# Kernel optimization log

Measured on AMD Instinct MI355X. Metric: run time of the kernel, lower is better.

The kernel has to match this reference:

```python
import jax, jax.numpy as jnp
import numpy as np

H = 16           # num_heads
D = 1024         # num_units
QD = KD = VD = 64
LN_EPS = 1e-5


def _xavier(key, shape):
    fan_in, fan_out = shape[-2], shape[-1]
    std = np.sqrt(2.0 / (fan_in + fan_out))
    return jax.random.normal(key, shape, dtype=jnp.float32) * std


def setup_inputs() -> dict:
    key = jax.random.key(0)
    ks = jax.random.split(key, 10)
    B, Sq, Sk = 8, 1024, 1024
    return {
        "query": jax.random.normal(ks[0], (B, Sq, D), dtype=jnp.float32),
        "keys": jax.random.normal(ks[1], (B, Sk, D), dtype=jnp.float32),
        "values": jax.random.normal(ks[2], (B, Sk, D), dtype=jnp.float32),
        "Wq": _xavier(ks[3], (H, D, QD)),
        "Wk": _xavier(ks[4], (H, D, KD)),
        "Wv": _xavier(ks[5], (H, D, VD)),
        "Wp": _xavier(ks[6], (H * VD, D)),   # proj, stored input-major: y = x @ Wp + bp
        "bp": jnp.zeros((D,), dtype=jnp.float32),
        "gamma": jnp.ones((D,), dtype=jnp.float32),
        "beta": jnp.zeros((D,), dtype=jnp.float32),
    }


def reference(query, keys, values, Wq, Wk, Wv, Wp, bp, gamma, beta):
    B, Sq, _ = query.shape
    Sk = keys.shape[1]
    # RepeatLinear per head: [B,S,D] x [H,D,e] -> [H,B,S,e]
    Q = jnp.einsum("bsd,hde->hbse", query, Wq)
    K = jnp.einsum("bsd,hde->hbse", keys, Wk)
    V = jnp.einsum("bsd,hde->hbse", values, Wv)
    # NOTE: original scales by sqrt(num_units), not sqrt(key_dim)
    temper = jnp.asarray(np.sqrt(D), dtype=Q.dtype)
    scores = jnp.einsum("hbqe,hbke->hbqk", Q, K) / temper  # [H,B,Sq,Sk]
    attn = jax.nn.softmax(scores, axis=-1)
    # dropout is identity in eval mode
    out = jnp.einsum("hbqk,hbke->hbqe", attn, V)           # [H,B,Sq,VD]
    # torch.cat(torch.split(out, B, 0), -1): head-major feature concat
    out = out.transpose(1, 2, 0, 3).reshape(B, Sq, H * VD)
    out = out @ Wp + bp                                     # proj
    # residual + LayerNorm
    y = out + query
    mu = jnp.mean(y, axis=-1, keepdims=True)
    var = jnp.var(y, axis=-1, keepdims=True)
    y = (y - mu) / jnp.sqrt(var + LN_EPS) * gamma + beta
    return y, attn.reshape(H * B, Sq, Sk)
```

## Files before the change

### kernel.cpp

```cpp
#include <hip/hip_runtime.h>
#include <hip/hip_bf16.h>

#define H_ 16
#define B_ 8
#define S_ 1024
#define D_ 1024
#define E_ 64
#define HB_ 128
#define LN_EPS 1e-5f

typedef unsigned short u16;
typedef __bf16 bf16x8 __attribute__((ext_vector_type(8)));
typedef u16 u16x8 __attribute__((ext_vector_type(8)));
typedef u16 u16x4 __attribute__((ext_vector_type(4)));
typedef float f32x4 __attribute__((ext_vector_type(4)));

#define MFMA16(a, b, c) __builtin_amdgcn_mfma_f32_16x16x32_bf16( \
    __builtin_bit_cast(bf16x8, (a)), __builtin_bit_cast(bf16x8, (b)), (c), 0, 0, 0)

#define GLL16(gp, lp) __builtin_amdgcn_global_load_lds( \
    (const __attribute__((address_space(1))) void*)(gp), \
    (__attribute__((address_space(3))) void*)(lp), 16, 0, 0)

__device__ __forceinline__ u16 f2bf(float x) {
  union { float f; unsigned u; } v; v.f = x;
  unsigned r = v.u + 0x7fffu + ((v.u >> 16) & 1u);
  return (u16)(r >> 16);
}

__global__ __launch_bounds__(256) void k_transpose_all(
    const float* __restrict__ Wq, const float* __restrict__ Wk,
    const float* __restrict__ Wv, const float* __restrict__ Wp,
    u16* __restrict__ Wt) {
  __shared__ float tile[64][65];
  const int bid = blockIdx.x;
  const int which = bid >> 8, r = bid & 255;
  const float* src;
  int R, C, rt, ct;
  float scale = 1.0f;
  size_t soff, doff;
  if (which < 3) {
    src = which == 0 ? Wq : which == 1 ? Wk : Wv;
    if (which == 0) scale = 1.0f / 32.0f;
    int slice = r & 15, rtile = r >> 4;
    R = 1024; C = 64; rt = rtile * 64; ct = 0;
    soff = (size_t)slice * 65536;
    doff = (size_t)which * (1 << 20) + (size_t)slice * 65536;
  } else {
    src = Wp;
    R = 1024; C = 1024; rt = (r & 15) * 64; ct = (r >> 4) * 64;
    soff = 0; doff = (size_t)3 * (1 << 20);
  }
  const float* I = src + soff;
  u16* O = Wt + doff;
  const int t = threadIdx.x;
  const int c4 = (t & 15) * 4;
  #pragma unroll
  for (int i = 0; i < 4; i++) {
    int rr = i * 16 + (t >> 4);
    f32x4 v = *(const f32x4*)&I[(size_t)(rt + rr) * C + ct + c4];
    tile[rr][c4 + 0] = v[0]; tile[rr][c4 + 1] = v[1];
    tile[rr][c4 + 2] = v[2]; tile[rr][c4 + 3] = v[3];
  }
  __syncthreads();
  #pragma unroll
  for (int i = 0; i < 4; i++) {
    int oc = i * 16 + (t >> 4);
    u16x4 v;
    #pragma unroll
    for (int rr = 0; rr < 4; rr++) v[rr] = f2bf(tile[c4 + rr][oc] * scale);
    *(u16x4*)&O[(size_t)(ct + oc) * R + rt + c4] = v;
  }
}

__global__ void k_convert3(const float* __restrict__ Xq, const float* __restrict__ Xk,
    const float* __restrict__ Xv, u16* __restrict__ dst) {
  const int bid = blockIdx.x;
  const int t = bid >> 12;
  const float* X = t == 0 ? Xq : t == 1 ? Xk : Xv;
  u16* Y = dst + (size_t)t * (8 << 20);
  int i = ((bid & 4095) * 256 + threadIdx.x) * 8;
  float4 a = *(const float4*)(X + i);
  float4 b = *(const float4*)(X + i + 4);
  u16x8 v;
  v[0] = f2bf(a.x); v[1] = f2bf(a.y); v[2] = f2bf(a.z); v[3] = f2bf(a.w);
  v[4] = f2bf(b.x); v[5] = f2bf(b.y); v[6] = f2bf(b.z); v[7] = f2bf(b.w);
  *(u16x8*)(Y + i) = v;
}

#define STAGE_TILES() do { \
    GLL16(Ag + kt,             AsB0); \
    GLL16(Ag + 64 * 1024 + kt, AsB0 + 2048); \
    GLL16(Bg + kt,             BsB0); \
    GLL16(Bg + 64 * 1024 + kt, BsB0 + 2048); \
  } while (0)

#define READ_FRAGS() do { \
    _Pragma("unroll") \
    for (int mi = 0; mi < 4; mi++) \
      af[mi] = *(const u16x8*)&As[(wr * 64 + mi * 16 + lr) * 32 + lg * 8]; \
    _Pragma("unroll") \
    for (int ni = 0; ni < 4; ni++) \
      bf[ni] = *(const u16x8*)&Bs[(wc * 64 + ni * 16 + lr) * 32 + lg * 8]; \
  } while (0)

template<int MODE>
__global__ __launch_bounds__(256) void k_gemm(
    const u16* __restrict__ X0, const u16* __restrict__ Ball,
    u16* __restrict__ O0, u16* __restrict__ O1, u16* __restrict__ O2,
    float* __restrict__ Pf, const float* __restrict__ bp,
    const float* __restrict__ query) {
  const int bid = blockIdx.x + (blockIdx.y << 6);
  const int bx  = ((bid & 7) << 3) + ((bid >> 3) & 7);
  const int by  = bid >> 6;
  const int l  = threadIdx.x & 63;
  const int w  = threadIdx.x >> 6;
  const int lr = l & 15, lg = l >> 4;
  const int wr = w >> 1, wc = w & 1;
  const int m0 = bx * 128, n0 = by * 128;

  const u16* A = (MODE == 0) ? X0 + (size_t)(by >> 3) * (8 << 20) : X0;

  __shared__ __align__(16) u16 As[128 * 32];
  __shared__ __align__(16) u16 Bs[128 * 32];

  const int srow = w * 16 + (l >> 2);
  const int scol = (l & 3) * 8;
  const u16* Ag = A    + (size_t)(m0 + srow) * 1024 + scol;
  const u16* Bg = Ball + (size_t)(n0 + srow) * 1024 + scol;
  u16* AsB0 = As + w * 512;
  u16* BsB0 = Bs + w * 512;

  f32x4 acc[4][4] = {};
  u16x8 af[4], bf[4];

  if (MODE == 2 || by < 16) {
    for (int kt = 0; kt < 1024; kt += 32) {
      STAGE_TILES();
      __syncthreads();
      READ_FRAGS();
      #pragma unroll
      for (int mi = 0; mi < 4; mi++)
        #pragma unroll
        for (int ni = 0; ni < 4; ni++)
          acc[mi][ni] = MFMA16(bf[ni], af[mi], acc[mi][ni]);
      __syncthreads();
    }
  } else {
    for (int kt = 0; kt < 1024; kt += 32) {
      STAGE_TILES();
      __syncthreads();
      READ_FRAGS();
      #pragma unroll
      for (int mi = 0; mi < 4; mi++)
        #pragma unroll
        for (int ni = 0; ni < 4; ni++)
          acc[mi][ni] = MFMA16(af[mi], bf[ni], acc[mi][ni]);
      __syncthreads();
    }
  }

  if (MODE == 0 && by < 16) {
    u16* Out = (by >= 8) ? O1 : O0;
    const int h = (by & 7) * 2 + wc;
    #pragma unroll
    for (int mi = 0; mi < 4; mi++) {
      int s = m0 + wr * 64 + mi * 16 + lr;
      int bb = s >> 10, ss = s & 1023;
      #pragma unroll
      for (int ni = 0; ni < 4; ni++) {
        u16x4 v;
        #pragma unroll
        for (int r = 0; r < 4; r++) v[r] = f2bf(acc[mi][ni][r]);
        *(u16x4*)&Out[((size_t)(h * 8 + bb) * 1024 + ss) * 64 + ni * 16 + lg * 4] = v;
      }
    }
  } else if (MODE == 0) {
    const int byv = by - 16;
    const int h = byv * 2 + wc;
    #pragma unroll
    for (int mi = 0; mi < 4; mi++) {
      int s = m0 + wr * 64 + mi * 16 + lg * 4;
      int bb = s >> 10, ss = s & 1023;
      #pragma unroll
      for (int ni = 0; ni < 4; ni++) {
        u16x4 v;
        #pragma unroll
        for (int r = 0; r < 4; r++) v[r] = f2bf(acc[mi][ni][r]);
        *(u16x4*)&O2[((size_t)(h * 8 + bb) * 64 + ni * 16 + lr) * 1024 + ss] = v;
      }
    }
  } else {
    #pragma unroll
    for (int mi = 0; mi < 4; mi++) {
      int m = m0 + wr * 64 + mi * 16 + lr;
      #pragma unroll
      for (int ni = 0; ni < 4; ni++) {
        int n = n0 + wc * 64 + ni * 16 + lg * 4;
        f32x4 b4 = *(const f32x4*)(bp + n);
        f32x4 q4 = *(const f32x4*)(query + (size_t)m * 1024 + n);
        f32x4 o = acc[mi][ni] + b4 + q4;
        *(f32x4*)(Pf + (size_t)m * 1024 + n) = o;
      }
    }
  }
}

__global__ __launch_bounds__(256, 4) void k_attn(const u16* __restrict__ Qb,
    const u16* __restrict__ Kb, const u16* __restrict__ Vtb,
    float* __restrict__ attn_out, u16* __restrict__ AO) {
  const int bid = blockIdx.x;
  const int xcd = bid & 7, within = bid >> 3;
  const int qt = within & 63;
  const int hb = xcd * 16 + (within >> 6);
  const int w  = threadIdx.x >> 6;
  const int l  = threadIdx.x & 63;
  const int lr = l & 15, lg = l >> 4;
  const int q0 = qt * 16;

  __shared__ __align__(16) u16 pbuf[16 * 1024];
  __shared__ float wmaxs[4][16];
  __shared__ float wsums[4][16];

  const u16* Qp = Qb + ((size_t)hb * 1024 + q0 + lr) * 64 + lg * 8;
  const u16* Kp = Kb + ((size_t)hb * 1024 + w * 256 + lr) * 64 + lg * 8;
  u16x8 q_lo = *(const u16x8*)Qp;
  u16x8 q_hi = *(const u16x8*)(Qp + 32);

  f32x4 sacc[16] = {};
  __builtin_amdgcn_s_setprio(1);
  #pragma unroll
  for (int j = 0; j < 16; j++) {
    u16x8 k0 = *(const u16x8*)(Kp + (size_t)j * 16 * 64);
    u16x8 k1 = *(const u16x8*)(Kp + (size_t)j * 16 * 64 + 32);
    sacc[j] = MFMA16(k0, q_lo, sacc[j]);
    sacc[j] = MFMA16(k1, q_hi, sacc[j]);
  }
  __builtin_amdgcn_s_setprio(0);

  float mx = sacc[0][0];
  #pragma unroll
  for (int j = 0; j < 16; j++)
    #pragma unroll
    for (int r = 0; r < 4; r++) mx = fmaxf(mx, sacc[j][r]);
  mx = fmaxf(mx, __shfl_xor(mx, 16));
  mx = fmaxf(mx, __shfl_xor(mx, 32));

  float sum = 0.f;
  #pragma unroll
  for (int j = 0; j < 16; j++)
    #pragma unroll
    for (int r = 0; r < 4; r++) {
      float p = __expf(sacc[j][r] - mx);
      sacc[j][r] = p;
      sum += p;
    }
  sum += __shfl_xor(sum, 16);
  sum += __shfl_xor(sum, 32);

  const u16* Vp = Vtb + ((size_t)hb * 64 + w * 16 + lr) * 1024 + lg * 8;
  u16x8 vp0 = *(const u16x8*)(Vp + 0);
  u16x8 vp1 = *(const u16x8*)(Vp + 32);
  u16x8 vp2 = *(const u16x8*)(Vp + 64);
  u16x8 vp3 = *(const u16x8*)(Vp + 96);

  #pragma unroll
  for (int j = 0; j < 16; j++) {
    u16x4 pb;
    #pragma unroll
    for (int r = 0; r < 4; r++) pb[r] = f2bf(sacc[j][r]);
    int k0 = w * 256 + j * 16 + lg * 4;
    int byte = (lr * 2048 + k0 * 2) ^ ((lr & 7) << 4);
    *(u16x4*)((char*)pbuf + byte) = pb;
  }
  if (l < 16) { wmaxs[w][lr] = mx; wsums[w][lr] = sum; }

  __syncthreads();

  float m0v = wmaxs[0][lr], m1v = wmaxs[1][lr], m2v = wmaxs[2][lr], m3v = wmaxs[3][lr];
  float gmax = fmaxf(fmaxf(m0v, m1v), fmaxf(m2v, m3v));
  float e0 = __expf(m0v - gmax), e1 = __expf(m1v - gmax);
  float e2 = __expf(m2v - gmax), e3 = __expf(m3v - gmax);
  float gsum = wsums[0][lr] * e0 + wsums[1][lr] * e1 + wsums[2][lr] * e2 + wsums[3][lr] * e3;
  float inv = 1.0f / gsum;
  float c0 = e0 * inv, c1 = e1 * inv, c2 = e2 * inv, c3 = e3 * inv;
  float scale_own = __expf(mx - gmax) * inv;

  float* Ap = attn_out + ((size_t)hb * 1024 + q0 + lr) * 1024 + w * 256 + lg * 4;
  #pragma unroll
  for (int j = 0; j < 16; j++) {
    f32x4 v = sacc[j] * scale_own;
    __builtin_nontemporal_store(v, (f32x4*)(Ap + j * 16));
  }

  f32x4 o0 = {}, o1 = {}, o2 = {}, o3 = {};
  __builtin_amdgcn_s_setprio(1);
  #pragma unroll
  for (int i = 0; i < 4; i++)
    #pragma unroll
    for (int kk = 0; kk < 8; kk++) {
      int kb = i * 256 + kk * 32 + lg * 8;
      int byte = (lr * 2048 + kb * 2) ^ ((lr & 7) << 4);
      u16x8 p = *(u16x8*)((char*)pbuf + byte);
      u16x8 v;
      if (i == 0 && kk == 0) v = vp0;
      else if (i == 0 && kk == 1) v = vp1;
      else if (i == 0 && kk == 2) v = vp2;
      else if (i == 0 && kk == 3) v = vp3;
      else v = *(const u16x8*)(Vp + i * 256 + kk * 32);
      if (i == 0) o0 = MFMA16(v, p, o0);
      else if (i == 1) o1 = MFMA16(v, p, o1);
      else if (i == 2) o2 = MFMA16(v, p, o2);
      else o3 = MFMA16(v, p, o3);
    }
  __builtin_amdgcn_s_setprio(0);

  const int bb = hb & 7, hh = hb >> 3;
  u16x4 ov;
  #pragma unroll
  for (int r = 0; r < 4; r++)
    ov[r] = f2bf(o0[r] * c0 + o1[r] * c1 + o2[r] * c2 + o3[r] * c3);
  *(u16x4*)&AO[((size_t)bb * 1024 + q0 + lr) * 1024 + hh * 64 + w * 16 + lg * 4] = ov;
}

__global__ __launch_bounds__(256) void k_ln(const float* __restrict__ P,
    const float* __restrict__ gamma, const float* __restrict__ beta,
    float* __restrict__ y) {
  const int row = blockIdx.x * 4 + (threadIdx.x >> 6);
  const int l = threadIdx.x & 63;
  const float* p = P + (size_t)row * 1024 + l * 4;
  f32x4 v[4];
  float s = 0.f, s2 = 0.f;
  #pragma unroll
  for (int i = 0; i < 4; i++) {
    v[i] = *(const f32x4*)(p + i * 256);
    #pragma unroll
    for (int r = 0; r < 4; r++) { s += v[i][r]; s2 += v[i][r] * v[i][r]; }
  }
  #pragma unroll
  for (int off = 1; off < 64; off <<= 1) {
    s += __shfl_xor(s, off);
    s2 += __shfl_xor(s2, off);
  }
  float mu = s * (1.0f / 1024.0f);
  float var = s2 * (1.0f / 1024.0f) - mu * mu;
  float rstd = rsqrtf(var + LN_EPS);
  float* yp = y + (size_t)row * 1024 + l * 4;
  #pragma unroll
  for (int i = 0; i < 4; i++) {
    f32x4 g = *(const f32x4*)(gamma + l * 4 + i * 256);
    f32x4 b = *(const f32x4*)(beta + l * 4 + i * 256);
    f32x4 o;
    #pragma unroll
    for (int r = 0; r < 4; r++) o[r] = (v[i][r] - mu) * rstd * g[r] + b[r];
    __builtin_nontemporal_store(o, (f32x4*)(yp + i * 256));
  }
}

extern "C" void kernel_launch(void* const* d_in, const int* in_sizes, int n_in,
                              void* d_out, int out_size, void* d_ws, size_t ws_size,
                              hipStream_t stream) {
  const float* query  = (const float*)d_in[0];
  const float* keys   = (const float*)d_in[1];
  const float* values = (const float*)d_in[2];
  const float* Wq     = (const float*)d_in[3];
  const float* Wk     = (const float*)d_in[4];
  const float* Wv     = (const float*)d_in[5];
  const float* Wp     = (const float*)d_in[6];
  const float* bp     = (const float*)d_in[7];
  const float* gamma  = (const float*)d_in[8];
  const float* beta   = (const float*)d_in[9];

  float* y        = (float*)d_out;
  float* attn_out = (float*)d_out + (size_t)B_ * S_ * D_;

  u16* ws  = (u16*)d_ws;
  u16* Wqt = ws;
  u16* Wvt = Wqt + (2 << 20);
  u16* Wpt = Wqt + (3 << 20);
  u16* Xqb = Wqt + (4 << 20);
  u16* Xvb = Xqb + (16 << 20);
  u16* Qb  = Xqb + (24 << 20);
  u16* Kb  = Qb + (8 << 20);
  u16* Vtb = Kb + (8 << 20);
  u16* AO  = Vtb + (8 << 20);
  float* P = (float*)Xqb;
  (void)Wvt;

  k_transpose_all<<<1024, 256, 0, stream>>>(Wq, Wk, Wv, Wp, Wqt);
  k_convert3<<<12288, 256, 0, stream>>>(query, keys, values, Xqb);

  k_gemm<0><<<dim3(64, 24), 256, 0, stream>>>(Xqb, Wqt, Qb, Kb, Vtb, nullptr, nullptr, nullptr);

  k_attn<<<8192, 256, 0, stream>>>(Qb, Kb, Vtb, attn_out, AO);

  k_gemm<2><<<dim3(64, 8), 256, 0, stream>>>(AO, Wpt, nullptr, nullptr, nullptr, P, bp, query);
  k_ln<<<2048, 256, 0, stream>>>(P, gamma, beta, y);
}
```

Measured before the change: 421.9 us.

## Split attention into score/softmax kernel and separate tiled P·V GEMM

Splits the fused attention kernel into two. The first computes scores and softmax, then writes both the fp32 attention output and a bf16 copy of the probabilities to workspace. The second kernel runs P·V as a tiled GEMM using LDS loads. This removes each block's repeated V read and its large LDS staging buffer, but adds a full bf16 probability round trip through global memory plus an extra launch.

```diff
diff --git a/kernel.cpp b/kernel.cpp
--- a/kernel.cpp
+++ b/kernel.cpp
@@ -206,9 +206,8 @@
   }
 }
 
-__global__ __launch_bounds__(256, 4) void k_attn(const u16* __restrict__ Qb,
-    const u16* __restrict__ Kb, const u16* __restrict__ Vtb,
-    float* __restrict__ attn_out, u16* __restrict__ AO) {
+__global__ __launch_bounds__(256, 4) void k_score(const u16* __restrict__ Qb,
+    const u16* __restrict__ Kb, float* __restrict__ attn_out, u16* __restrict__ Pws) {
   const int bid = blockIdx.x;
   const int xcd = bid & 7, within = bid >> 3;
   const int qt = within & 63;
@@ -218,7 +217,6 @@
   const int lr = l & 15, lg = l >> 4;
   const int q0 = qt * 16;
 
-  __shared__ __align__(16) u16 pbuf[16 * 1024];
   __shared__ float wmaxs[4][16];
   __shared__ float wsums[4][16];
 
@@ -258,69 +256,87 @@
   sum += __shfl_xor(sum, 16);
   sum += __shfl_xor(sum, 32);
 
-  const u16* Vp = Vtb + ((size_t)hb * 64 + w * 16 + lr) * 1024 + lg * 8;
-  u16x8 vp0 = *(const u16x8*)(Vp + 0);
-  u16x8 vp1 = *(const u16x8*)(Vp + 32);
-  u16x8 vp2 = *(const u16x8*)(Vp + 64);
-  u16x8 vp3 = *(const u16x8*)(Vp + 96);
-
-  #pragma unroll
-  for (int j = 0; j < 16; j++) {
-    u16x4 pb;
-    #pragma unroll
-    for (int r = 0; r < 4; r++) pb[r] = f2bf(sacc[j][r]);
-    int k0 = w * 256 + j * 16 + lg * 4;
-    int byte = (lr * 2048 + k0 * 2) ^ ((lr & 7) << 4);
-    *(u16x4*)((char*)pbuf + byte) = pb;
-  }
   if (l < 16) { wmaxs[w][lr] = mx; wsums[w][lr] = sum; }
-
   __syncthreads();
 
   float m0v = wmaxs[0][lr], m1v = wmaxs[1][lr], m2v = wmaxs[2][lr], m3v = wmaxs[3][lr];
   float gmax = fmaxf(fmaxf(m0v, m1v), fmaxf(m2v, m3v));
-  float e0 = __expf(m0v - gmax), e1 = __expf(m1v - gmax);
-  float e2 = __expf(m2v - gmax), e3 = __expf(m3v - gmax);
-  float gsum = wsums[0][lr] * e0 + wsums[1][lr] * e1 + wsums[2][lr] * e2 + wsums[3][lr] * e3;
-  float inv = 1.0f / gsum;
-  float c0 = e0 * inv, c1 = e1 * inv, c2 = e2 * inv, c3 = e3 * inv;
-  float scale_own = __expf(mx - gmax) * inv;
+  float gsum = wsums[0][lr] * __expf(m0v - gmax) + wsums[1][lr] * __expf(m1v - gmax)
+             + wsums[2][lr] * __expf(m2v - gmax) + wsums[3][lr] * __expf(m3v - gmax);
+  const float cown = __expf(mx - gmax) / gsum;
 
   float* Ap = attn_out + ((size_t)hb * 1024 + q0 + lr) * 1024 + w * 256 + lg * 4;
+  u16*   Pp = Pws + ((size_t)hb * 1024 + q0 + lr) * 1024 + w * 256 + lg * 4;
   #pragma unroll
   for (int j = 0; j < 16; j++) {
-    f32x4 v = sacc[j] * scale_own;
+    f32x4 v = sacc[j] * cown;
     __builtin_nontemporal_store(v, (f32x4*)(Ap + j * 16));
-  }
-
-  f32x4 o0 = {}, o1 = {}, o2 = {}, o3 = {};
-  __builtin_amdgcn_s_setprio(1);
-  #pragma unroll
-  for (int i = 0; i < 4; i++)
-    #pragma unroll
-    for (int kk = 0; kk < 8; kk++) {
-      int kb = i * 256 + kk * 32 + lg * 8;
-      int byte = (lr * 2048 + kb * 2) ^ ((lr & 7) << 4);
-      u16x8 p = *(u16x8*)((char*)pbuf + byte);
-      u16x8 v;
-      if (i == 0 && kk == 0) v = vp0;
-      else if (i == 0 && kk == 1) v = vp1;
-      else if (i == 0 && kk == 2) v = vp2;
-      else if (i == 0 && kk == 3) v = vp3;
-      else v = *(const u16x8*)(Vp + i * 256 + kk * 32);
-      if (i == 0) o0 = MFMA16(v, p, o0);
-      else if (i == 1) o1 = MFMA16(v, p, o1);
-      else if (i == 2) o2 = MFMA16(v, p, o2);
-      else o3 = MFMA16(v, p, o3);
-    }
-  __builtin_amdgcn_s_setprio(0);
+    u16x4 pb;
+    #pragma unroll
+    for (int r = 0; r < 4; r++) pb[r] = f2bf(v[r]);
+    *(u16x4*)(Pp + j * 16) = pb;
+  }
+}
+
+__global__ __launch_bounds__(256) void k_pv(const u16* __restrict__ Pws,
+    const u16* __restrict__ Vtb, u16* __restrict__ AO) {
+  const int bid = blockIdx.x;
+  const int xcd = bid & 7, within = bid >> 3;
+  const int mt = within & 7;
+  const int hb = xcd * 16 + (within >> 3);
+  const int l  = threadIdx.x & 63;
+  const int w  = threadIdx.x >> 6;
+  const int lr = l & 15, lg = l >> 4;
+  const int wr = w >> 1, wc = w & 1;
+  const int m0 = mt * 128;
+
+  __shared__ __align__(16) u16 As[128 * 32];
+  __shared__ __align__(16) u16 Bs[64 * 32];
+
+  const int srow = w * 16 + (l >> 2);
+  const int scol = (l & 3) * 8;
+  const u16* Ag = Pws + ((size_t)hb * 1024 + m0 + srow) * 1024 + scol;
+  const u16* Bg = Vtb + ((size_t)hb * 64 + srow) * 1024 + scol;
+  u16* AsB0 = As + w * 512;
+  u16* BsB0 = Bs + w * 512;
+
+  f32x4 acc[4][2] = {};
+
+  for (int kt = 0; kt < 1024; kt += 32) {
+    GLL16(Ag + kt,             AsB0);
+    GLL16(Ag + 64 * 1024 + kt, AsB0 + 2048);
+    GLL16(Bg + kt,             BsB0);
+    __syncthreads();
+
+    u16x8 af[4], bf[2];
+    #pragma unroll
+    for (int mi = 0; mi < 4; mi++)
+      af[mi] = *(const u16x8*)&As[(wr * 64 + mi * 16 + lr) * 32 + lg * 8];
+    #pragma unroll
+    for (int ni = 0; ni < 2; ni++)
+      bf[ni] = *(const u16x8*)&Bs[(wc * 32 + ni * 16 + lr) * 32 + lg * 8];
+
+    #pragma unroll
+    for (int mi = 0; mi < 4; mi++)
+      #pragma unroll
+      for (int ni = 0; ni < 2; ni++)
+        acc[mi][ni] = MFMA16(bf[ni], af[mi], acc[mi][ni]);
+    __syncthreads();
+  }
 
   const int bb = hb & 7, hh = hb >> 3;
-  u16x4 ov;
-  #pragma unroll
-  for (int r = 0; r < 4; r++)
-    ov[r] = f2bf(o0[r] * c0 + o1[r] * c1 + o2[r] * c2 + o3[r] * c3);
-  *(u16x4*)&AO[((size_t)bb * 1024 + q0 + lr) * 1024 + hh * 64 + w * 16 + lg * 4] = ov;
+  #pragma unroll
+  for (int mi = 0; mi < 4; mi++) {
+    int q = m0 + wr * 64 + mi * 16 + lr;
+    #pragma unroll
+    for (int ni = 0; ni < 2; ni++) {
+      int e = wc * 32 + ni * 16 + lg * 4;
+      u16x4 v;
+      #pragma unroll
+      for (int r = 0; r < 4; r++) v[r] = f2bf(acc[mi][ni][r]);
+      *(u16x4*)&AO[((size_t)bb * 1024 + q) * 1024 + hh * 64 + e] = v;
+    }
+  }
 }
 
 __global__ __launch_bounds__(256) void k_ln(const float* __restrict__ P,
@@ -376,23 +392,22 @@
 
   u16* ws  = (u16*)d_ws;
   u16* Wqt = ws;
-  u16* Wvt = Wqt + (2 << 20);
   u16* Wpt = Wqt + (3 << 20);
   u16* Xqb = Wqt + (4 << 20);
-  u16* Xvb = Xqb + (16 << 20);
   u16* Qb  = Xqb + (24 << 20);
   u16* Kb  = Qb + (8 << 20);
   u16* Vtb = Kb + (8 << 20);
   u16* AO  = Vtb + (8 << 20);
+  u16* Pws = AO + (8 << 20);
   float* P = (float*)Xqb;
-  (void)Wvt;
 
   k_transpose_all<<<1024, 256, 0, stream>>>(Wq, Wk, Wv, Wp, Wqt);
   k_convert3<<<12288, 256, 0, stream>>>(query, keys, values, Xqb);
 
   k_gemm<0><<<dim3(64, 24), 256, 0, stream>>>(Xqb, Wqt, Qb, Kb, Vtb, nullptr, nullptr, nullptr);
 
-  k_attn<<<8192, 256, 0, stream>>>(Qb, Kb, Vtb, attn_out, AO);
+  k_score<<<8192, 256, 0, stream>>>(Qb, Kb, attn_out, Pws);
+  k_pv<<<1024, 256, 0, stream>>>(Pws, Vtb, AO);
 
   k_gemm<2><<<dim3(64, 8), 256, 0, stream>>>(AO, Wpt, nullptr, nullptr, nullptr, P, bp, query);
   k_ln<<<2048, 256, 0, stream>>>(P, gamma, beta, y);
```

Result: slower. 500.7 us (+18.7%).
